# Performance work log

Measured on AMD Instinct MI355X. Metric: run time of the kernel, lower is better.

Reference implementation:

```python
import jax, jax.numpy as jnp
import numpy as np

B, C, H, W = 8, 256, 160, 160
CRED, GROUPS = 64, 8
EPS = 1e-4      # curvature eps (module arg)
GN_EPS = 1e-5   # torch GroupNorm default


def _depthwise3x3(y, k33):
    # y: [B,Cr,H,W]; k33: [3,3] fixed kernel applied per-channel
    k = jnp.broadcast_to(k33, (CRED, 1, 3, 3)).astype(y.dtype)
    return jax.lax.conv_general_dilated(
        y, k, window_strides=(1, 1), padding='SAME',
        feature_group_count=CRED,
        dimension_numbers=('NCHW', 'OIHW', 'NCHW'))


def setup_inputs() -> dict:
    key = jax.random.key(0)
    ks = jax.random.split(key, 6)
    return {
        'x': jax.random.normal(ks[0], (B, C, H, W), jnp.float32),
        'reduce_w': jax.random.normal(ks[1], (CRED, C, 1, 1), jnp.float32) * 0.05,
        'gn_scale': jnp.ones((CRED,), jnp.float32),
        'gn_bias': jnp.zeros((CRED,), jnp.float32),
        'gate_w1': jax.random.normal(ks[2], (16, CRED, 1, 1), jnp.float32) * 0.1,
        'gate_b1': jnp.zeros((16,), jnp.float32),
        'gate_w2': jax.random.normal(ks[3], (CRED, 16, 1, 1), jnp.float32) * 0.1,
        'gate_b2': jnp.zeros((CRED,), jnp.float32),
        'fuse_w': jax.random.normal(ks[4], (1, 2 * CRED, 1, 1), jnp.float32) * 0.1,
    }


def reference(x, reduce_w, gn_scale, gn_bias, gate_w1, gate_b1, gate_w2, gate_b2, fuse_w):
    b = x.shape[0]
    # 1x1 reduce conv (no bias)
    y = jnp.einsum('bchw,oc->bohw', x, reduce_w[:, :, 0, 0])
    # GroupNorm(8, 64)
    yg = y.reshape(b, GROUPS, CRED // GROUPS, H, W)
    mean = yg.mean(axis=(2, 3, 4), keepdims=True)
    var = yg.var(axis=(2, 3, 4), keepdims=True)
    y = ((yg - mean) * jax.lax.rsqrt(var + GN_EPS)).reshape(b, CRED, H, W)
    y = y * gn_scale[None, :, None, None] + gn_bias[None, :, None, None]
    # fixed depthwise convs: mean3, sobel-x, sobel-y
    mean_k = jnp.full((3, 3), 1.0 / 9.0, jnp.float32)
    sobel_x = jnp.array([[1., 0., -1.], [2., 0., -2.], [1., 0., -1.]], jnp.float32) / 4.0
    mu = _depthwise3x3(y, mean_k)
    gx = _depthwise3x3(y, sobel_x)
    gy = _depthwise3x3(y, sobel_x.T)
    # curvature elementwise chain
    ratio = jnp.clip(jnp.abs(y - mu) / (jnp.abs(gx) + jnp.abs(gy) + EPS), 0.0, 2.0)
    kappa = jnp.clip(1.0 - ratio, -1.0, 1.0)
    # SE-style gate on y: GAP -> 1x1 -> relu -> 1x1 -> sigmoid
    p = y.mean(axis=(2, 3))                                   # [B,Cr]
    hdn = jax.nn.relu(p @ gate_w1[:, :, 0, 0].T + gate_b1)    # [B,16]
    gamma = jax.nn.sigmoid(hdn @ gate_w2[:, :, 0, 0].T + gate_b2)  # [B,Cr]
    gated = gamma[:, :, None, None] * kappa
    # fuse: 1x1 conv over cat([kappa, gated]) -> sigmoid -> scale 0.1
    fw = fuse_w[0, :, 0, 0]
    a = jax.nn.sigmoid(jnp.einsum('bchw,c->bhw', kappa, fw[:CRED]) +
                       jnp.einsum('bchw,c->bhw', gated, fw[CRED:]))[:, None]
    return x * (1.0 + 0.1 * a)
```

## Files before the change

### kernel.cpp

```cpp
#include <hip/hip_runtime.h>
#include <hip/hip_bf16.h>
#include <math.h>

#define HW2D 25600
#define NB 8
#define NC 256
#define CR 64
#define H_ 160
#define W_ 160

typedef short bf16x8 __attribute__((ext_vector_type(8)));
typedef float f32x4 __attribute__((ext_vector_type(4)));

__device__ __forceinline__ short f2bf(float f) {
    __hip_bfloat16 h = __float2bfloat16(f);
    return *reinterpret_cast<short*>(&h);
}
__device__ __forceinline__ float bf2f(unsigned short b) {
    union { unsigned u; float f; } v; v.u = ((unsigned)b) << 16;
    return v.f;
}

__global__ __launch_bounds__(256) void k_pack(const float* __restrict__ rw,
                                              short* __restrict__ aPack) {
    int t = blockIdx.x * 256 + threadIdx.x;
    if (t >= 2048) return;
    int s = t >> 8, m = (t >> 6) & 3, lane = t & 63;
    int row = m * 16 + (lane & 15);
    int k0 = s * 32 + (lane >> 4) * 8;
    short* dst = aPack + ((size_t)((s * 4 + m) * 64 + lane)) * 8;
#pragma unroll
    for (int j = 0; j < 8; ++j)
        dst[j] = f2bf(rw[row * NC + k0 + j]);
}

__global__ __launch_bounds__(256) void k_rmfma(const float* __restrict__ x,
                                               const short* __restrict__ aPack,
                                               unsigned short* __restrict__ y0) {
    int wave = __builtin_amdgcn_readfirstlane(threadIdx.x >> 6);
    int lane = threadIdx.x & 63;
    int blk = blockIdx.x;
    int b = blk / 200;
    int pxb = (blk - b * 200) * 128 + wave * 32;
    int l15 = lane & 15, kg = lane >> 4;
    int laneoff = kg * 8 * HW2D + l15;
    const float* xw = x + (size_t)b * NC * HW2D + pxb;
    f32x4 acc[4][2];
    f32x4 zz = {0.f, 0.f, 0.f, 0.f};
#pragma unroll
    for (int m = 0; m < 4; ++m)
#pragma unroll
        for (int n = 0; n < 2; ++n) acc[m][n] = zz;
    const bf16x8* ap = (const bf16x8*)aPack + lane;
#pragma unroll
    for (int s = 0; s < 8; ++s) {
        bf16x8 a0 = ap[(s * 4 + 0) * 64];
        bf16x8 a1 = ap[(s * 4 + 1) * 64];
        bf16x8 a2 = ap[(s * 4 + 2) * 64];
        bf16x8 a3 = ap[(s * 4 + 3) * 64];
        const float* xs = xw + s * 32 * HW2D + laneoff;
        bf16x8 b0, b1;
#pragma unroll
        for (int j = 0; j < 8; ++j) {
            b0[j] = f2bf(xs[j * HW2D]);
            b1[j] = f2bf(xs[j * HW2D + 16]);
        }
        acc[0][0] = __builtin_amdgcn_mfma_f32_16x16x32_bf16(a0, b0, acc[0][0], 0, 0, 0);
        acc[0][1] = __builtin_amdgcn_mfma_f32_16x16x32_bf16(a0, b1, acc[0][1], 0, 0, 0);
        acc[1][0] = __builtin_amdgcn_mfma_f32_16x16x32_bf16(a1, b0, acc[1][0], 0, 0, 0);
        acc[1][1] = __builtin_amdgcn_mfma_f32_16x16x32_bf16(a1, b1, acc[1][1], 0, 0, 0);
        acc[2][0] = __builtin_amdgcn_mfma_f32_16x16x32_bf16(a2, b0, acc[2][0], 0, 0, 0);
        acc[2][1] = __builtin_amdgcn_mfma_f32_16x16x32_bf16(a2, b1, acc[2][1], 0, 0, 0);
        acc[3][0] = __builtin_amdgcn_mfma_f32_16x16x32_bf16(a3, b0, acc[3][0], 0, 0, 0);
        acc[3][1] = __builtin_amdgcn_mfma_f32_16x16x32_bf16(a3, b1, acc[3][1], 0, 0, 0);
    }
    unsigned short* yw = y0 + (size_t)b * CR * HW2D + pxb;
#pragma unroll
    for (int m = 0; m < 4; ++m)
#pragma unroll
        for (int n = 0; n < 2; ++n)
#pragma unroll
            for (int i = 0; i < 4; ++i) {
                int o = m * 16 + kg * 4 + i;
                yw[o * HW2D + n * 16 + l15] = (unsigned short)f2bf(acc[m][n][i]);
            }
}

__global__ __launch_bounds__(256) void k_stats(const unsigned short* __restrict__ y0,
                                               float* __restrict__ sum,
                                               float* __restrict__ sumsq) {
    int bc = blockIdx.x;
    const unsigned short* yp = y0 + (size_t)bc * HW2D;
    float s = 0.f, sq = 0.f;
    for (int i = threadIdx.x; i < HW2D / 8; i += 256) {
        const ushort4* p = (const ushort4*)(yp + i * 8);
        ushort4 v0 = p[0], v1 = p[1];
        float f0 = bf2f(v0.x), f1 = bf2f(v0.y), f2 = bf2f(v0.z), f3 = bf2f(v0.w);
        float f4 = bf2f(v1.x), f5 = bf2f(v1.y), f6 = bf2f(v1.z), f7 = bf2f(v1.w);
        s += (f0 + f1 + f2 + f3) + (f4 + f5 + f6 + f7);
        sq = fmaf(f0, f0, sq); sq = fmaf(f1, f1, sq);
        sq = fmaf(f2, f2, sq); sq = fmaf(f3, f3, sq);
        sq = fmaf(f4, f4, sq); sq = fmaf(f5, f5, sq);
        sq = fmaf(f6, f6, sq); sq = fmaf(f7, f7, sq);
    }
#pragma unroll
    for (int off = 32; off; off >>= 1) {
        s += __shfl_xor(s, off, 64);
        sq += __shfl_xor(sq, off, 64);
    }
    __shared__ float ls[4], lq[4];
    int wid = threadIdx.x >> 6;
    if ((threadIdx.x & 63) == 0) { ls[wid] = s; lq[wid] = sq; }
    __syncthreads();
    if (threadIdx.x == 0) {
        sum[bc]   = ls[0] + ls[1] + ls[2] + ls[3];
        sumsq[bc] = lq[0] + lq[1] + lq[2] + lq[3];
    }
}

__global__ __launch_bounds__(512) void k_gate(const float* __restrict__ sum,
                                              const float* __restrict__ sumsq,
                                              const float* __restrict__ gn_scale,
                                              const float* __restrict__ gn_bias,
                                              const float* __restrict__ w1,
                                              const float* __restrict__ b1,
                                              const float* __restrict__ w2,
                                              const float* __restrict__ b2,
                                              const float* __restrict__ fw,
                                              float* __restrict__ sA,
                                              float* __restrict__ sB,
                                              float* __restrict__ wef) {
    int t = threadIdx.x;
    int b = t >> 6, c = t & 63;
    __shared__ float sh_sum[512], sh_sq[512], sh_p[512], sh_h[128];
    float s = sum[t], sq = sumsq[t];
    sh_sum[t] = s;
    sh_sq[t] = sq;
    __syncthreads();
    int base = (t & ~7);
    float gs = 0.f, gq = 0.f;
#pragma unroll
    for (int i = 0; i < 8; ++i) { gs += sh_sum[base + i]; gq += sh_sq[base + i]; }
    const float invN = 1.0f / (8.0f * HW2D);
    float mean = gs * invN;
    float var = gq * invN - mean * mean;
    float rstd = rsqrtf(var + 1e-5f);
    float A = rstd * gn_scale[c];
    float Bv = gn_bias[c] - mean * A;
    sA[t] = A;
    sB[t] = Bv;
    float chmean = s * (1.0f / HW2D);
    sh_p[t] = chmean * A + Bv;
    __syncthreads();
    if (t < 128) {
        int bb = t >> 4, j = t & 15;
        float h = b1[j];
        for (int i = 0; i < 64; ++i) h = fmaf(sh_p[bb * 64 + i], w1[j * 64 + i], h);
        sh_h[t] = fmaxf(h, 0.f);
    }
    __syncthreads();
    float gacc = b2[c];
#pragma unroll
    for (int j = 0; j < 16; ++j) gacc = fmaf(sh_h[b * 16 + j], w2[c * 16 + j], gacc);
    float gamma = 1.0f / (1.0f + expf(-gacc));
    wef[t] = fw[c] + gamma * fw[CR + c];
}

__global__ __launch_bounds__(256) void k_stencil(const unsigned short* __restrict__ y0,
                                                 const float* __restrict__ sA,
                                                 const float* __restrict__ sB,
                                                 const float* __restrict__ wef,
                                                 float* __restrict__ pbuf) {
    const int tw = blockIdx.x * 32, th = blockIdx.y * 16;
    const int b = blockIdx.z & 7, q = blockIdx.z >> 3;
    const int c0 = q * 16;
    __shared__ float sm[2][18 * 36];
    int t = threadIdx.x;
    int col = t & 31, row0 = t >> 5;
    float logit0 = 0.f, logit1 = 0.f;
    const unsigned short* yb = y0 + (size_t)b * CR * HW2D;

    auto stage = [&](int c, int buf) {
        const unsigned short* yc = yb + (size_t)c * HW2D;
        float A = sA[b * 64 + c], Bv = sB[b * 64 + c];
        for (int i = t; i < 18 * 18; i += 256) {
            int r = i / 18, u = i - r * 18;
            int gh = th + r - 1;
            int gw0 = tw - 2 + u * 2;
            float s0 = 0.f, s1 = 0.f;
            if ((unsigned)gh < 160u) {
                const unsigned short* rowp = yc + gh * W_;
                if ((unsigned)gw0 < 159u) {
                    ushort2 v = *(const ushort2*)(rowp + gw0);
                    s0 = fmaf(A, bf2f(v.x), Bv);
                    s1 = fmaf(A, bf2f(v.y), Bv);
                } else {
                    if ((unsigned)gw0 < 160u)       s0 = fmaf(A, bf2f(rowp[gw0]), Bv);
                    if ((unsigned)(gw0 + 1) < 160u) s1 = fmaf(A, bf2f(rowp[gw0 + 1]), Bv);
                }
            }
            float* d = sm[buf] + r * 36 + u * 2;
            d[0] = s0;
            d[1] = s1;
        }
    };
    stage(c0, 0);
    __syncthreads();
    for (int ci = 0; ci < 16; ++ci) {
        int c = c0 + ci;
        if (ci < 15) stage(c + 1, (ci + 1) & 1);
        float wf = wef[b * 64 + c];
        const float* smc = sm[ci & 1];
#pragma unroll
        for (int k = 0; k < 2; ++k) {
            int r = row0 + k * 8;
            const float* p = smc + r * 36 + col + 1;
            float v00 = p[0],  v01 = p[1],  v02 = p[2];
            float v10 = p[36], v11 = p[37], v12 = p[38];
            float v20 = p[72], v21 = p[73], v22 = p[74];
            float mu = (v00 + v01 + v02 + v10 + v11 + v12 + v20 + v21 + v22) * (1.f / 9.f);
            float gx = (v00 - v02 + 2.f * (v10 - v12) + v20 - v22) * 0.25f;
            float gy = (v00 - v20 + 2.f * (v01 - v21) + v02 - v22) * 0.25f;
            float ratio = fminf(fabsf(v11 - mu) / (fabsf(gx) + fabsf(gy) + 1e-4f), 2.f);
            float kap = 1.f - ratio;
            if (k == 0) logit0 = fmaf(wf, kap, logit0);
            else        logit1 = fmaf(wf, kap, logit1);
        }
        __syncthreads();
    }
    float* pb = pbuf + ((size_t)q * NB + b) * HW2D;
    int r0 = th + row0, cpx = tw + col;
    pb[r0 * W_ + cpx]       = logit0;
    pb[(r0 + 8) * W_ + cpx] = logit1;
}

__global__ __launch_bounds__(256) void k_fuse(const float* __restrict__ pbuf,
                                              float* __restrict__ abuf) {
    int i = blockIdx.x * 256 + threadIdx.x;
    if (i >= NB * HW2D / 4) return;
    const float4* p4 = (const float4*)pbuf;
    float4 q0 = p4[i];
    float4 q1 = p4[2 * NB * HW2D / 4 - NB * HW2D / 4 + i];
    float4 q2 = p4[2 * NB * HW2D / 4 + i];
    float4 q3 = p4[3 * NB * HW2D / 4 + i];
    float4 a;
    a.x = 1.f / (1.f + expf(-(q0.x + q1.x + q2.x + q3.x)));
    a.y = 1.f / (1.f + expf(-(q0.y + q1.y + q2.y + q3.y)));
    a.z = 1.f / (1.f + expf(-(q0.z + q1.z + q2.z + q3.z)));
    a.w = 1.f / (1.f + expf(-(q0.w + q1.w + q2.w + q3.w)));
    ((float4*)abuf)[i] = a;
}

__global__ __launch_bounds__(256) void k_apply(const float* __restrict__ x,
                                               const float* __restrict__ abuf,
                                               float* __restrict__ out) {
    int px4 = blockIdx.x * 256 + threadIdx.x;
    int c = blockIdx.y, b = blockIdx.z;
    size_t xi = ((size_t)(b * NC + c)) * (HW2D / 4) + px4;
    float4 xv = ((const float4*)x)[xi];
    float4 av = ((const float4*)abuf)[b * (HW2D / 4) + px4];
    float4 ov;
    ov.x = xv.x * fmaf(0.1f, av.x, 1.f);
    ov.y = xv.y * fmaf(0.1f, av.y, 1.f);
    ov.z = xv.z * fmaf(0.1f, av.z, 1.f);
    ov.w = xv.w * fmaf(0.1f, av.w, 1.f);
    ((float4*)out)[xi] = ov;
}

extern "C" void kernel_launch(void* const* d_in, const int* in_sizes, int n_in,
                              void* d_out, int out_size, void* d_ws, size_t ws_size,
                              hipStream_t stream) {
    const float* x   = (const float*)d_in[0];
    const float* rw  = (const float*)d_in[1];
    const float* gns = (const float*)d_in[2];
    const float* gnb = (const float*)d_in[3];
    const float* w1  = (const float*)d_in[4];
    const float* b1  = (const float*)d_in[5];
    const float* w2  = (const float*)d_in[6];
    const float* b2  = (const float*)d_in[7];
    const float* fw  = (const float*)d_in[8];
    float* out = (float*)d_out;

    float* ws    = (float*)d_ws;
    float* pbuf  = ws;
    float* abuf  = pbuf + 4 * (size_t)NB * HW2D;
    float* sum   = abuf + (size_t)NB * HW2D;
    float* sumsq = sum + 512;
    float* sA    = sumsq + 512;
    float* sB    = sA + 512;
    float* wef   = sB + 512;
    short* aPack = (short*)(wef + 512);
    unsigned short* y0 = (unsigned short*)(aPack + 16384);

    hipLaunchKernelGGL(k_pack,    dim3(8),          dim3(256), 0, stream, rw, aPack);
    hipLaunchKernelGGL(k_rmfma,   dim3(1600),       dim3(256), 0, stream, x, aPack, y0);
    hipLaunchKernelGGL(k_stats,   dim3(512),        dim3(256), 0, stream, y0, sum, sumsq);
    hipLaunchKernelGGL(k_gate,    dim3(1),          dim3(512), 0, stream,
                       sum, sumsq, gns, gnb, w1, b1, w2, b2, fw, sA, sB, wef);
    hipLaunchKernelGGL(k_stencil, dim3(5, 10, 32),  dim3(256), 0, stream, y0, sA, sB, wef, pbuf);
    hipLaunchKernelGGL(k_fuse,    dim3(200),        dim3(256), 0, stream, pbuf, abuf);
    hipLaunchKernelGGL(k_apply,   dim3(25, 256, 8), dim3(256), 0, stream, x, abuf, out);
}
```

Before: 173.1 us.

## Fuse stencil, sigmoid fuse and apply into one tail kernel

Replaces the channel-split stencil kernel, the partial-logit reduction kernel and the elementwise apply kernel with one kernel. Each block processes all 64 reduced channels for an 8x32 tile, computes the sigmoid gate in shared memory, then scales all 256 input channels for that tile. This removes the partial-logit buffer round trip and two launches. In exchange the grid shrinks from 1600 to 800 blocks, each stencil block runs a longer serial channel loop, and the x/out streaming is done by those same blocks, which may cut parallelism for the bandwidth-bound apply phase.

```diff
diff --git a/kernel.cpp b/kernel.cpp
--- a/kernel.cpp
+++ b/kernel.cpp
@@ -166,25 +166,25 @@
     wef[t] = fw[c] + gamma * fw[CR + c];
 }
 
-__global__ __launch_bounds__(256) void k_stencil(const unsigned short* __restrict__ y0,
-                                                 const float* __restrict__ sA,
-                                                 const float* __restrict__ sB,
-                                                 const float* __restrict__ wef,
-                                                 float* __restrict__ pbuf) {
-    const int tw = blockIdx.x * 32, th = blockIdx.y * 16;
-    const int b = blockIdx.z & 7, q = blockIdx.z >> 3;
-    const int c0 = q * 16;
-    __shared__ float sm[2][18 * 36];
-    int t = threadIdx.x;
-    int col = t & 31, row0 = t >> 5;
-    float logit0 = 0.f, logit1 = 0.f;
+__global__ __launch_bounds__(256) void k_tail(const unsigned short* __restrict__ y0,
+                                              const float* __restrict__ x,
+                                              const float* __restrict__ sA,
+                                              const float* __restrict__ sB,
+                                              const float* __restrict__ wef,
+                                              float* __restrict__ out) {
+    const int tw = blockIdx.x * 32, th = blockIdx.y * 8, b = blockIdx.z;
+    __shared__ float sm[2][10 * 36];
+    __shared__ float av[256];
+    const int t = threadIdx.x;
+    const int col = t & 31, row = t >> 5;
+    float logit = 0.f;
     const unsigned short* yb = y0 + (size_t)b * CR * HW2D;
 
     auto stage = [&](int c, int buf) {
-        const unsigned short* yc = yb + (size_t)c * HW2D;
-        float A = sA[b * 64 + c], Bv = sB[b * 64 + c];
-        for (int i = t; i < 18 * 18; i += 256) {
-            int r = i / 18, u = i - r * 18;
+        if (t < 180) {
+            const unsigned short* yc = yb + (size_t)c * HW2D;
+            float A = sA[b * 64 + c], Bv = sB[b * 64 + c];
+            int r = t / 18, u = t - r * 18;
             int gh = th + r - 1;
             int gw0 = tw - 2 + u * 2;
             float s0 = 0.f, s1 = 0.f;
@@ -204,67 +204,41 @@
             d[1] = s1;
         }
     };
-    stage(c0, 0);
-    __syncthreads();
-    for (int ci = 0; ci < 16; ++ci) {
-        int c = c0 + ci;
-        if (ci < 15) stage(c + 1, (ci + 1) & 1);
+    stage(0, 0);
+    __syncthreads();
+    for (int c = 0; c < CR; ++c) {
+        if (c < CR - 1) stage(c + 1, (c + 1) & 1);
         float wf = wef[b * 64 + c];
-        const float* smc = sm[ci & 1];
-#pragma unroll
-        for (int k = 0; k < 2; ++k) {
-            int r = row0 + k * 8;
-            const float* p = smc + r * 36 + col + 1;
-            float v00 = p[0],  v01 = p[1],  v02 = p[2];
-            float v10 = p[36], v11 = p[37], v12 = p[38];
-            float v20 = p[72], v21 = p[73], v22 = p[74];
-            float mu = (v00 + v01 + v02 + v10 + v11 + v12 + v20 + v21 + v22) * (1.f / 9.f);
-            float gx = (v00 - v02 + 2.f * (v10 - v12) + v20 - v22) * 0.25f;
-            float gy = (v00 - v20 + 2.f * (v01 - v21) + v02 - v22) * 0.25f;
-            float ratio = fminf(fabsf(v11 - mu) / (fabsf(gx) + fabsf(gy) + 1e-4f), 2.f);
-            float kap = 1.f - ratio;
-            if (k == 0) logit0 = fmaf(wf, kap, logit0);
-            else        logit1 = fmaf(wf, kap, logit1);
-        }
+        const float* p = sm[c & 1] + row * 36 + col + 1;
+        float v00 = p[0],  v01 = p[1],  v02 = p[2];
+        float v10 = p[36], v11 = p[37], v12 = p[38];
+        float v20 = p[72], v21 = p[73], v22 = p[74];
+        float mu = (v00 + v01 + v02 + v10 + v11 + v12 + v20 + v21 + v22) * (1.f / 9.f);
+        float gx = (v00 - v02 + 2.f * (v10 - v12) + v20 - v22) * 0.25f;
+        float gy = (v00 - v20 + 2.f * (v01 - v21) + v02 - v22) * 0.25f;
+        float ratio = fminf(fabsf(v11 - mu) / (fabsf(gx) + fabsf(gy) + 1e-4f), 2.f);
+        float kap = 1.f - ratio;
+        logit = fmaf(wf, kap, logit);
         __syncthreads();
     }
-    float* pb = pbuf + ((size_t)q * NB + b) * HW2D;
-    int r0 = th + row0, cpx = tw + col;
-    pb[r0 * W_ + cpx]       = logit0;
-    pb[(r0 + 8) * W_ + cpx] = logit1;
-}
-
-__global__ __launch_bounds__(256) void k_fuse(const float* __restrict__ pbuf,
-                                              float* __restrict__ abuf) {
-    int i = blockIdx.x * 256 + threadIdx.x;
-    if (i >= NB * HW2D / 4) return;
-    const float4* p4 = (const float4*)pbuf;
-    float4 q0 = p4[i];
-    float4 q1 = p4[2 * NB * HW2D / 4 - NB * HW2D / 4 + i];
-    float4 q2 = p4[2 * NB * HW2D / 4 + i];
-    float4 q3 = p4[3 * NB * HW2D / 4 + i];
-    float4 a;
-    a.x = 1.f / (1.f + expf(-(q0.x + q1.x + q2.x + q3.x)));
-    a.y = 1.f / (1.f + expf(-(q0.y + q1.y + q2.y + q3.y)));
-    a.z = 1.f / (1.f + expf(-(q0.z + q1.z + q2.z + q3.z)));
-    a.w = 1.f / (1.f + expf(-(q0.w + q1.w + q2.w + q3.w)));
-    ((float4*)abuf)[i] = a;
-}
-
-__global__ __launch_bounds__(256) void k_apply(const float* __restrict__ x,
-                                               const float* __restrict__ abuf,
-                                               float* __restrict__ out) {
-    int px4 = blockIdx.x * 256 + threadIdx.x;
-    int c = blockIdx.y, b = blockIdx.z;
-    size_t xi = ((size_t)(b * NC + c)) * (HW2D / 4) + px4;
-    float4 xv = ((const float4*)x)[xi];
-    float4 av = ((const float4*)abuf)[b * (HW2D / 4) + px4];
-    float4 ov;
-    ov.x = xv.x * fmaf(0.1f, av.x, 1.f);
-    ov.y = xv.y * fmaf(0.1f, av.y, 1.f);
-    ov.z = xv.z * fmaf(0.1f, av.z, 1.f);
-    ov.w = xv.w * fmaf(0.1f, av.w, 1.f);
-    ((float4*)out)[xi] = ov;
+    av[t] = fmaf(0.1f, 1.f / (1.f + expf(-logit)), 1.f);
+    __syncthreads();
+
+    const int slot = t & 63, chg = t >> 6;
+    const int row_s = slot >> 3, cg = slot & 7;
+    float4 a4 = ((const float4*)av)[slot];
+    const size_t pbase = (size_t)b * NC * HW2D + (size_t)(th + row_s) * W_ + tw + cg * 4;
+#pragma unroll 4
+    for (int it = 0; it < 64; ++it) {
+        size_t xi = pbase + (size_t)(it * 4 + chg) * HW2D;
+        float4 xv = *(const float4*)(x + xi);
+        float4 ov;
+        ov.x = xv.x * a4.x;
+        ov.y = xv.y * a4.y;
+        ov.z = xv.z * a4.z;
+        ov.w = xv.w * a4.w;
+        *(float4*)(out + xi) = ov;
+    }
 }
 
 extern "C" void kernel_launch(void* const* d_in, const int* in_sizes, int n_in,
@@ -282,9 +256,7 @@
     float* out = (float*)d_out;
 
     float* ws    = (float*)d_ws;
-    float* pbuf  = ws;
-    float* abuf  = pbuf + 4 * (size_t)NB * HW2D;
-    float* sum   = abuf + (size_t)NB * HW2D;
+    float* sum   = ws;
     float* sumsq = sum + 512;
     float* sA    = sumsq + 512;
     float* sB    = sA + 512;
@@ -292,12 +264,11 @@
     short* aPack = (short*)(wef + 512);
     unsigned short* y0 = (unsigned short*)(aPack + 16384);
 
-    hipLaunchKernelGGL(k_pack,    dim3(8),          dim3(256), 0, stream, rw, aPack);
-    hipLaunchKernelGGL(k_rmfma,   dim3(1600),       dim3(256), 0, stream, x, aPack, y0);
-    hipLaunchKernelGGL(k_stats,   dim3(512),        dim3(256), 0, stream, y0, sum, sumsq);
-    hipLaunchKernelGGL(k_gate,    dim3(1),          dim3(512), 0, stream,
+    hipLaunchKernelGGL(k_pack,  dim3(8),         dim3(256), 0, stream, rw, aPack);
+    hipLaunchKernelGGL(k_rmfma, dim3(1600),      dim3(256), 0, stream, x, aPack, y0);
+    hipLaunchKernelGGL(k_stats, dim3(512),       dim3(256), 0, stream, y0, sum, sumsq);
+    hipLaunchKernelGGL(k_gate,  dim3(1),         dim3(512), 0, stream,
                        sum, sumsq, gns, gnb, w1, b1, w2, b2, fw, sA, sB, wef);
-    hipLaunchKernelGGL(k_stencil, dim3(5, 10, 32),  dim3(256), 0, stream, y0, sA, sB, wef, pbuf);
-    hipLaunchKernelGGL(k_fuse,    dim3(200),        dim3(256), 0, stream, pbuf, abuf);
-    hipLaunchKernelGGL(k_apply,   dim3(25, 256, 8), dim3(256), 0, stream, x, abuf, out);
-}
+    hipLaunchKernelGGL(k_tail,  dim3(5, 20, 8),  dim3(256), 0, stream,
+                       y0, x, sA, sB, wef, out);
+}
```

Result: slower. 227.8 us (+31.6%).
